# Kernel tuning notes

Measured on AMD Instinct MI355X. Metric: run time of the kernel, lower is better.

The kernel has to match this reference:

```python
import jax, jax.numpy as jnp
import numpy as np

P = 4          # patch_size
LAM = 0.5      # init_lambda
B, C, H, W = 8, 96, 128, 128

def _dct_mat(N):
    # torch_dct unnormalized DCT-II matrix: D[k,n] = 2*cos(pi*(2n+1)k/(2N))
    n = np.arange(N)
    return 2.0 * np.cos(np.pi * (2.0 * n[None, :] + 1.0) * n[:, None] / (2.0 * N))

_D = jnp.asarray(_dct_mat(P), dtype=jnp.float32)
_Di = jnp.asarray(np.linalg.inv(_dct_mat(P)), dtype=jnp.float32)  # exact inverse -> idct(dct(x)) == x

def _dct2(x):
    # DCT-II over last two dims of [..., P, P]
    return jnp.einsum('ij,...jk,lk->...il', _D, x, _D)

def _idct2(x):
    return jnp.einsum('ij,...jk,lk->...il', _Di, x, _Di)

def _conv3x3(x, w, b):
    y = jax.lax.conv_general_dilated(x, w, (1, 1), 'SAME',
                                     dimension_numbers=('NCHW', 'OIHW', 'NCHW'))
    return y + b[None, :, None, None]

def setup_inputs() -> dict:
    key = jax.random.key(0)
    ks = jax.random.split(key, 5)
    std = 1.0 / np.sqrt(C * 9)
    return {
        'input1': jax.random.normal(ks[0], (B, C, H, W), jnp.float32),
        'input2': jax.random.normal(ks[1], (B, C, H, W), jnp.float32),
        'wq': jax.random.normal(ks[2], (C, C, 3, 3), jnp.float32) * std,
        'bq': jnp.zeros((C,), jnp.float32),
        'wk': jax.random.normal(ks[3], (C, C, 3, 3), jnp.float32) * std,
        'bk': jnp.zeros((C,), jnp.float32),
        'wv': jax.random.normal(ks[4], (C, C, 3, 3), jnp.float32) * std,
        'bv': jnp.zeros((C,), jnp.float32),
        'temperature': jnp.ones((1, 1), jnp.float32),
    }

def reference(input1, input2, wq, bq, wk, bk, wv, bv, temperature):
    b, c, h, w = input1.shape
    F_Q = _conv3x3(input1, wq, bq)
    F_K = _conv3x3(input1, wk, bk)
    F_V = _conv3x3(input2, wv, bv)
    hp, wp = h // P, w // P
    # 'b c (h p1) (w p2) -> b c h w p1 p2'
    to_patch = lambda x: x.reshape(b, c, hp, P, wp, P).transpose(0, 1, 2, 4, 3, 5)
    fft_Q = _dct2(to_patch(F_Q))          # [b,c,hp,wp,P,P]
    fft_K = _dct2(to_patch(F_K))
    F1 = jnp.matmul(fft_Q, fft_K)         # per-patch PxP matmul
    L = hp * wp * P * P                   # == h*w
    F1f = F1.reshape(b, c, L)
    Fq = fft_Q.reshape(b, c, L)
    Fk = fft_K.reshape(b, c, L)
    # channel-channel attention: [b,c,L] @ [b,L,c] -> [b,c,c]
    attn = jnp.einsum('bil,bjl->bij', Fq, Fk) * temperature[0, 0]
    attn = jax.nn.softmax(attn, axis=-1)
    Fcfr = jnp.einsum('bij,bjl->bil', attn, F1f).reshape(b, c, hp, wp, P, P)
    Fcfr_out = _idct2(Fcfr)
    # 'b c h w p1 p2 -> b c (h p1) (w p2)'
    Fcfrout = Fcfr_out.transpose(0, 1, 2, 4, 3, 5).reshape(b, c, h, w)
    out1 = jnp.matmul(Fcfrout, F_V)       # batched HxW matmul (H==W)
    Fdfr = F_V - out1 * LAM
    return jnp.matmul(Fcfrout, F_Q) + Fdfr
```

## Files before the change

kernel.cpp:

```cpp
#include <hip/hip_runtime.h>

typedef unsigned short u16;
typedef unsigned int u32;
typedef __bf16 bf16x8 __attribute__((ext_vector_type(8)));
typedef float f32x4 __attribute__((ext_vector_type(4)));
typedef int i32x4 __attribute__((ext_vector_type(4)));

#define BATCH 8
#define CH 96
#define HWSZ 16384
#define PADP (130*130*96)

#define OFF_FQ     0ULL
#define OFF_FK     50331648ULL
#define OFF_GT     50331648ULL
#define OFF_FVN    75497472ULL
#define OFF_PAD1H  100663296ULL
#define OFF_F1W    100663296ULL
#define OFF_PAD1L  126621696ULL
#define OFF_PART   126621696ULL
#define OFF_PAD2   152580096ULL
#define OFF_FCFR   152580096ULL
#define OFF_FVB    178538496ULL
#define OFF_ATTNB  203704320ULL
#define OFF_WQK    203851776ULL
#define OFF_WV     204515328ULL
#define WS_NEED    204681216ULL

__device__ __forceinline__ u16 f2bf(float f) {
    u32 u = __builtin_bit_cast(u32, f);
    u += 0x7fffu + ((u >> 16) & 1u);
    return (u16)(u >> 16);
}
__device__ __forceinline__ float bf2f(u16 h) {
    u32 u = ((u32)h) << 16;
    return __builtin_bit_cast(float, u);
}
__device__ __forceinline__ f32x4 mfma16(i32x4 a, i32x4 b, f32x4 c) {
    return __builtin_amdgcn_mfma_f32_16x16x32_bf16(
        __builtin_bit_cast(bf16x8, a), __builtin_bit_cast(bf16x8, b), c, 0, 0, 0);
}
__device__ __forceinline__ void gl_lds16(const u16* g, u16* l) {
    __builtin_amdgcn_global_load_lds(
        (const __attribute__((address_space(1))) unsigned int*)g,
        (__attribute__((address_space(3))) unsigned int*)l, 16, 0, 0);
}

__global__ __launch_bounds__(256) void k_diag(float* __restrict__ out, int n, float val) {
    for (int i = blockIdx.x * 256 + threadIdx.x; i < n; i += gridDim.x * 256) out[i] = val;
}

__global__ __launch_bounds__(256) void k_zhalo(u16* __restrict__ p) {
    size_t base = (size_t)blockIdx.x * PADP;
    for (int i = threadIdx.x; i < 130 * 96; i += 256) {
        p[base + i] = 0;
        p[base + (size_t)129 * 130 * 96 + i] = 0;
    }
    for (int i = threadIdx.x; i < 128 * 2 * 96; i += 256) {
        int row = i / 192, k = i - row * 192;
        int x = (k < 96) ? 0 : 129, c = (k < 96) ? k : k - 96;
        p[base + ((size_t)(row + 1) * 130 + x) * 96 + c] = 0;
    }
}

__global__ __launch_bounds__(256) void k_trans_split(const float* __restrict__ src,
        u16* __restrict__ dh, u16* __restrict__ dl) {
    __shared__ float tile[96][129];
    int b = blockIdx.x >> 7, y = blockIdx.x & 127;
    const float* s = src + (size_t)b * CH * HWSZ + (size_t)y * 128;
    for (int idx = threadIdx.x; idx < CH * 128; idx += 256) {
        int c = idx >> 7, x = idx & 127;
        tile[c][x] = s[(size_t)c * HWSZ + x];
    }
    __syncthreads();
    size_t obase = ((size_t)(b * 130 + y + 1) * 130 + 1) * 96;
    for (int idx = threadIdx.x; idx < 128 * CH; idx += 256) {
        int x = idx / CH, c = idx - x * CH;
        float v = tile[c][x];
        u16 h = f2bf(v);
        dh[obase + idx] = h;
        if (dl) dl[obase + idx] = f2bf(v - bf2f(h));
    }
}

__global__ __launch_bounds__(128) void k_weights_qk(const float* __restrict__ wq,
        const float* __restrict__ wk, u16* __restrict__ dst) {
    int co = blockIdx.x;
    const float* w = (co < 96) ? wq : wk;
    int cs = (co < 96) ? co : co - 96;
    for (int idx = threadIdx.x; idx < 864; idx += 128) {
        int tap = idx / 96, ci = idx - tap * 96;
        int cic = ci >> 5, g = (ci >> 3) & 3, c7 = ci & 7;
        float v = w[((size_t)cs * 96 + ci) * 9 + tap];
        u16 h = f2bf(v), lo = f2bf(v - bf2f(h));
        size_t s = (size_t)(cic * 9 + tap);
        dst[(((s * 2 + 0) * 4 + g) * 192 + co) * 8 + c7] = h;
        dst[(((s * 2 + 1) * 4 + g) * 192 + co) * 8 + c7] = lo;
    }
}

__global__ __launch_bounds__(128) void k_weights_v(const float* __restrict__ wv,
        u16* __restrict__ dst) {
    int co = blockIdx.x;
    for (int idx = threadIdx.x; idx < 864; idx += 128) {
        int tap = idx / 96, ci = idx - tap * 96;
        int cic = ci >> 5, g = (ci >> 3) & 3, c7 = ci & 7;
        float v = wv[((size_t)co * 96 + ci) * 9 + tap];
        size_t s = (size_t)(cic * 9 + tap);
        dst[((s * 4 + g) * 96 + co) * 8 + c7] = f2bf(v);
    }
}

__global__ __launch_bounds__(256, 3) void k_convqk2(
        const u16* __restrict__ ph, const u16* __restrict__ pl,
        const u16* __restrict__ wqk,
        const float* __restrict__ bq, const float* __restrict__ bk,
        float* __restrict__ fq, float* __restrict__ fk) {
    __shared__ u16 wbuf[2][12288];
    const int tid = threadIdx.x;
    const int b = blockIdx.x >> 7, y = blockIdx.x & 127;
    const int w = tid >> 6, lane = tid & 63, l15 = lane & 15, g = lane >> 4;
    f32x4 acc[2][12];
#pragma unroll
    for (int mf = 0; mf < 2; mf++)
#pragma unroll
        for (int f = 0; f < 12; f++) acc[mf][f] = (f32x4){0.f, 0.f, 0.f, 0.f};

    {
        u16* ldsb = &wbuf[0][0] + (size_t)w * 64 * 8;
#pragma unroll
        for (int j = 0; j < 6; j++)
            gl_lds16(wqk + (size_t)(j * 256 + tid) * 8, ldsb + (size_t)j * 256 * 8);
    }
    __syncthreads();
    for (int s = 0; s < 27; s++) {
        const int cur = s & 1;
        if (s + 1 < 27) {
            const u16* src = wqk + (size_t)(s + 1) * 12288;
            u16* ldsb = &wbuf[cur ^ 1][0] + (size_t)w * 64 * 8;
#pragma unroll
            for (int j = 0; j < 6; j++)
                gl_lds16(src + (size_t)(j * 256 + tid) * 8, ldsb + (size_t)j * 256 * 8);
        }
        const int cic = s / 9, tap = s - cic * 9;
        const int dy = tap / 3 - 1, dx = tap - (tap / 3) * 3 - 1;
        const int ci0 = cic * 32 + g * 8;
        size_t ab = ((size_t)(b * 130 + y + 1 + dy) * 130 + (w * 32 + l15 + 1 + dx)) * 96 + ci0;
        i32x4 ah0 = *(const i32x4*)(ph + ab);
        i32x4 ah1 = *(const i32x4*)(ph + ab + 16 * 96);
        i32x4 al0 = *(const i32x4*)(pl + ab);
        i32x4 al1 = *(const i32x4*)(pl + ab + 16 * 96);
#pragma unroll
        for (int f = 0; f < 12; f++) {
            i32x4 bh = *(const i32x4*)(&wbuf[cur][((0 + g) * 192 + f * 16 + l15) * 8]);
            i32x4 bl = *(const i32x4*)(&wbuf[cur][((4 + g) * 192 + f * 16 + l15) * 8]);
            acc[0][f] = mfma16(ah0, bh, acc[0][f]);
            acc[0][f] = mfma16(ah0, bl, acc[0][f]);
            acc[0][f] = mfma16(al0, bh, acc[0][f]);
            acc[1][f] = mfma16(ah1, bh, acc[1][f]);
            acc[1][f] = mfma16(ah1, bl, acc[1][f]);
            acc[1][f] = mfma16(al1, bh, acc[1][f]);
        }
        __syncthreads();
    }
#pragma unroll
    for (int f = 0; f < 12; f++) {
        const bool isQ = (f < 6);
        const int co = (isQ ? f : f - 6) * 16 + l15;
        const float bb = isQ ? bq[co] : bk[co];
        float* op = isQ ? fq : fk;
#pragma unroll
        for (int mf = 0; mf < 2; mf++) {
            const int xp = w * 32 + mf * 16 + g * 4;
#pragma unroll
            for (int r = 0; r < 4; r++)
                op[((size_t)((b * 128 + y) * 128 + xp + r)) * 96 + co] = acc[mf][f][r] + bb;
        }
    }
}

__global__ __launch_bounds__(256) void k_convv2(
        const u16* __restrict__ p2, const u16* __restrict__ wv,
        const float* __restrict__ bv, u16* __restrict__ fvb) {
    __shared__ u16 vbuf[2][3072];
    const int tid = threadIdx.x;
    const int b = blockIdx.x >> 7, y = blockIdx.x & 127;
    const int w = tid >> 6, lane = tid & 63, l15 = lane & 15, g = lane >> 4;
    f32x4 acc[2][6];
#pragma unroll
    for (int mf = 0; mf < 2; mf++)
#pragma unroll
        for (int f = 0; f < 6; f++) acc[mf][f] = (f32x4){0.f, 0.f, 0.f, 0.f};
    {
        gl_lds16(wv + (size_t)tid * 8, &vbuf[0][0] + (size_t)w * 64 * 8);
        if (w < 2)
            gl_lds16(wv + (size_t)(256 + tid) * 8, &vbuf[0][0] + (size_t)(256 + w * 64) * 8);
    }
    __syncthreads();
    for (int s = 0; s < 27; s++) {
        const int cur = s & 1;
        if (s + 1 < 27) {
            const u16* src = wv + (size_t)(s + 1) * 3072;
            gl_lds16(src + (size_t)tid * 8, &vbuf[cur ^ 1][0] + (size_t)w * 64 * 8);
            if (w < 2)
                gl_lds16(src + (size_t)(256 + tid) * 8, &vbuf[cur ^ 1][0] + (size_t)(256 + w * 64) * 8);
        }
        const int cic = s / 9, tap = s - cic * 9;
        const int dy = tap / 3 - 1, dx = tap - (tap / 3) * 3 - 1;
        const int ci0 = cic * 32 + g * 8;
        size_t ab = ((size_t)(b * 130 + y + 1 + dy) * 130 + (w * 32 + l15 + 1 + dx)) * 96 + ci0;
        i32x4 ah0 = *(const i32x4*)(p2 + ab);
        i32x4 ah1 = *(const i32x4*)(p2 + ab + 16 * 96);
#pragma unroll
        for (int f = 0; f < 6; f++) {
            i32x4 bfr = *(const i32x4*)(&vbuf[cur][(g * 96 + f * 16 + l15) * 8]);
            acc[0][f] = mfma16(ah0, bfr, acc[0][f]);
            acc[1][f] = mfma16(ah1, bfr, acc[1][f]);
        }
        __syncthreads();
    }
#pragma unroll
    for (int f = 0; f < 6; f++) {
        const int co = f * 16 + l15;
        const float bb = bv[co];
#pragma unroll
        for (int mf = 0; mf < 2; mf++) {
            const int xp = w * 32 + mf * 16 + g * 4;
#pragma unroll
            for (int r = 0; r < 4; r++)
                fvb[((size_t)((b * 128 + y) * 128 + xp + r)) * 96 + co] = f2bf(acc[mf][f][r] + bb);
        }
    }
}

__global__ __launch_bounds__(256) void k_patch(
        const float* __restrict__ fq, float* __restrict__ fk, u16* __restrict__ f1w) {
    int blk = blockIdx.x;
    int b = blk >> 6, py = (blk >> 1) & 31, xh = blk & 1;
    int y0 = py * 4;
    for (int it = 0; it < 6; it++) {
        int item = threadIdx.x + it * 256;
        int pxl = item / 96, c = item - pxl * 96;
        int x0 = (xh * 16 + pxl) * 4;
        float A[4][4], Bm[4][4];
        size_t rb[4];
#pragma unroll
        for (int r = 0; r < 4; r++) {
            rb[r] = ((size_t)((b * 128 + y0 + r) * 128 + x0)) * 96 + c;
#pragma unroll
            for (int m = 0; m < 4; m++) {
                A[r][m] = fq[rb[r] + (size_t)m * 96];
                Bm[r][m] = fk[rb[r] + (size_t)m * 96];
            }
        }
        float rsB[4], csB[4], rsA[4], tot = 0.f;
#pragma unroll
        for (int r = 0; r < 4; r++) {
            rsB[r] = Bm[r][0] + Bm[r][1] + Bm[r][2] + Bm[r][3];
            rsA[r] = A[r][0] + A[r][1] + A[r][2] + A[r][3];
            tot += rsB[r];
        }
#pragma unroll
        for (int m = 0; m < 4; m++) csB[m] = Bm[0][m] + Bm[1][m] + Bm[2][m] + Bm[3][m];
#pragma unroll
        for (int r = 0; r < 4; r++)
#pragma unroll
            for (int m = 0; m < 4; m++)
                fk[rb[r] + (size_t)m * 96] = 64.f * Bm[r][m] + 16.f * (rsB[r] + csB[m]) + 4.f * tot;
#pragma unroll
        for (int r = 0; r < 4; r++)
#pragma unroll
            for (int m = 0; m < 4; m++) {
                float ab = A[r][0] * Bm[0][m] + A[r][1] * Bm[1][m]
                         + A[r][2] * Bm[2][m] + A[r][3] * Bm[3][m];
                f1w[rb[r] + (size_t)m * 96] = f2bf(8.f * ab + 2.f * rsA[r] * csB[m]);
            }
    }
}

__global__ __launch_bounds__(256) void k_attn(
        const float* __restrict__ fq, const float* __restrict__ kt,
        float* __restrict__ part) {
    __shared__ float qs[96 * 65];
    __shared__ float ks[96 * 65];
    int b = blockIdx.x >> 6, s = blockIdx.x & 63;
    int l0 = s * 256;
    int tx = threadIdx.x & 15, ty = threadIdx.x >> 4;
    double accD[6][6];
#pragma unroll
    for (int a = 0; a < 6; a++)
#pragma unroll
        for (int bb = 0; bb < 6; bb++) accD[a][bb] = 0.0;
    for (int ch = 0; ch < 4; ch++) {
        __syncthreads();
        for (int idx = threadIdx.x; idx < 1536; idx += 256) {
            int p = idx / 24, c0 = (idx - p * 24) * 4;
            size_t off = ((size_t)b * 16384 + l0 + ch * 64 + p) * 96 + c0;
            f32x4 qv = *(const f32x4*)(fq + off);
            f32x4 kv = *(const f32x4*)(kt + off);
#pragma unroll
            for (int u = 0; u < 4; u++) {
                qs[(c0 + u) * 65 + p] = qv[u];
                ks[(c0 + u) * 65 + p] = kv[u];
            }
        }
        __syncthreads();
        float acc[6][6];
#pragma unroll
        for (int a = 0; a < 6; a++)
#pragma unroll
            for (int bb = 0; bb < 6; bb++) acc[a][bb] = 0.f;
        for (int l = 0; l < 64; l++) {
            float qv[6], kv[6];
#pragma unroll
            for (int a = 0; a < 6; a++) qv[a] = qs[(ty + 16 * a) * 65 + l];
#pragma unroll
            for (int bb = 0; bb < 6; bb++) kv[bb] = ks[(tx + 16 * bb) * 65 + l];
#pragma unroll
            for (int a = 0; a < 6; a++)
#pragma unroll
                for (int bb = 0; bb < 6; bb++) acc[a][bb] += qv[a] * kv[bb];
        }
#pragma unroll
        for (int a = 0; a < 6; a++)
#pragma unroll
            for (int bb = 0; bb < 6; bb++) accD[a][bb] += (double)acc[a][bb];
    }
#pragma unroll
    for (int a = 0; a < 6; a++)
#pragma unroll
        for (int bb = 0; bb < 6; bb++)
            part[((size_t)((b * 64 + s) * 96 + ty + 16 * a)) * 96 + tx + 16 * bb] = (float)accD[a][bb];
}

__global__ __launch_bounds__(128) void k_softmax(
        const float* __restrict__ part, const float* __restrict__ temp,
        u16* __restrict__ attnb) {
    __shared__ float red[128];
    int b = blockIdx.x / 96, i2 = blockIdx.x - b * 96;
    int j2 = threadIdx.x;
    float v = 0.f;
    if (j2 < 96) {
        for (int s = 0; s < 64; s++)
            v += part[((size_t)((b * 64 + s) * 96 + i2)) * 96 + j2];
        v *= temp[0];
    }
    red[j2] = (j2 < 96) ? v : -3.4e38f;
    __syncthreads();
    for (int off = 64; off >= 1; off >>= 1) {
        if (j2 < off) red[j2] = fmaxf(red[j2], red[j2 + off]);
        __syncthreads();
    }
    float mx = red[0];
    __syncthreads();
    float e = (j2 < 96) ? expf(v - mx) : 0.f;
    red[j2] = e;
    __syncthreads();
    for (int off = 64; off >= 1; off >>= 1) {
        if (j2 < off) red[j2] += red[j2 + off];
        __syncthreads();
    }
    float sum = red[0];
    if (j2 < 96) attnb[((size_t)(b * 96) + i2) * 96 + j2] = f2bf(e / sum);
}

__global__ __launch_bounds__(256) void k_gprep(
        const float* __restrict__ fqn, const u16* __restrict__ fvb,
        u16* __restrict__ gt, u16* __restrict__ fvn) {
    __shared__ u16 lg[8 * 32 * 33];
    __shared__ u16 lv[8 * 32 * 33];
    int blk = blockIdx.x;
    int b = blk / 192;
    int r = blk - b * 192;
    int yt = r / 48; r -= yt * 48;
    int xt = r / 12; int cc = r - xt * 12;
    int y0 = yt * 32, x0 = xt * 32, c0 = cc * 8;
    for (int idx = threadIdx.x; idx < 8192; idx += 256) {
        int pix = idx >> 3, cl = idx & 7;
        int yy = pix >> 5, xx = pix & 31;
        size_t off = ((size_t)((b * 128 + y0 + yy) * 128 + x0 + xx)) * 96 + c0 + cl;
        float q = fqn[off];
        float v = bf2f(fvb[off]);
        int la = (cl * 32 + yy) * 33 + xx;
        lg[la] = f2bf(q - 0.5f * v);
        lv[la] = f2bf(v);
    }
    __syncthreads();
    for (int idx = threadIdx.x; idx < 8192; idx += 256) {
        int yy = idx & 31, xl = (idx >> 5) & 31, cl = idx >> 10;
        gt[((size_t)((b * 96 + c0 + cl) * 128 + x0 + xl)) * 128 + y0 + yy] = lg[(cl * 32 + yy) * 33 + xl];
    }
    for (int idx = threadIdx.x; idx < 8192; idx += 256) {
        int xx = idx & 31, yl = (idx >> 5) & 31, cl = idx >> 10;
        fvn[((size_t)((b * 96 + c0 + cl) * 128 + y0 + yl)) * 128 + x0 + xx] = lv[(cl * 32 + yl) * 33 + xx];
    }
}

__global__ __launch_bounds__(256) void k_fcfr2(
        const u16* __restrict__ attnb, const u16* __restrict__ f1w,
        u16* __restrict__ fc) {
    int b = blockIdx.x >> 6, pc = blockIdx.x & 63;
    int lane = threadIdx.x & 63, wv_ = threadIdx.x >> 6;
    int l15 = lane & 15, g = lane >> 4;
    int pbase = pc * 256 + wv_ * 64;
    f32x4 acc[6][4];
#pragma unroll
    for (int m = 0; m < 6; m++)
#pragma unroll
        for (int n = 0; n < 4; n++) acc[m][n] = (f32x4){0.f, 0.f, 0.f, 0.f};
#pragma unroll
    for (int ks = 0; ks < 3; ks++) {
        int k0 = ks * 32 + g * 8;
        i32x4 afr[6];
#pragma unroll
        for (int m = 0; m < 6; m++)
            afr[m] = *(const i32x4*)(attnb + ((size_t)(b * 96 + m * 16 + l15)) * 96 + k0);
#pragma unroll
        for (int n = 0; n < 4; n++) {
            i32x4 bfr = *(const i32x4*)(f1w + ((size_t)(b * 16384 + pbase + n * 16 + l15)) * 96 + k0);
#pragma unroll
            for (int m = 0; m < 6; m++)
                acc[m][n] = mfma16(afr[m], bfr, acc[m][n]);
        }
    }
#pragma unroll
    for (int m = 0; m < 6; m++)
#pragma unroll
        for (int n = 0; n < 4; n++)
#pragma unroll
            for (int r = 0; r < 4; r++) {
                int i2 = m * 16 + g * 4 + r;
                int pix = pbase + n * 16 + l15;
                fc[((size_t)(b * 96 + i2)) * HWSZ + pix] = f2bf(acc[m][n][r]);
            }
}

__global__ __launch_bounds__(256) void k_final(
        const u16* __restrict__ fc, const u16* __restrict__ gt,
        const u16* __restrict__ fvn, float* __restrict__ out) {
    int b = blockIdx.x / 96, c = blockIdx.x - b * 96;
    int lane = threadIdx.x & 63, wv_ = threadIdx.x >> 6;
    int l15 = lane & 15, g = lane >> 4;
    const u16* A = fc + ((size_t)(b * 96 + c)) * HWSZ;
    const u16* Bm = gt + ((size_t)(b * 96 + c)) * HWSZ;
    f32x4 acc[2][8];
#pragma unroll
    for (int mf = 0; mf < 2; mf++)
#pragma unroll
        for (int nf = 0; nf < 8; nf++) acc[mf][nf] = (f32x4){0.f, 0.f, 0.f, 0.f};
#pragma unroll
    for (int kc = 0; kc < 4; kc++) {
        int k0 = kc * 32 + g * 8;
        i32x4 af[2];
#pragma unroll
        for (int mf = 0; mf < 2; mf++)
            af[mf] = *(const i32x4*)(A + (size_t)(wv_ * 32 + mf * 16 + l15) * 128 + k0);
#pragma unroll
        for (int nf = 0; nf < 8; nf++) {
            i32x4 bf = *(const i32x4*)(Bm + (size_t)(nf * 16 + l15) * 128 + k0);
#pragma unroll
            for (int mf = 0; mf < 2; mf++)
                acc[mf][nf] = mfma16(af[mf], bf, acc[mf][nf]);
        }
    }
    const u16* V = fvn + ((size_t)(b * 96 + c)) * HWSZ;
    float* O = out + ((size_t)(b * 96 + c)) * HWSZ;
#pragma unroll
    for (int mf = 0; mf < 2; mf++)
#pragma unroll
        for (int nf = 0; nf < 8; nf++)
#pragma unroll
            for (int r = 0; r < 4; r++) {
                int y = wv_ * 32 + mf * 16 + g * 4 + r;
                int x = nf * 16 + l15;
                O[y * 128 + x] = acc[mf][nf][r] + bf2f(V[y * 128 + x]);
            }
}

extern "C" void kernel_launch(void* const* d_in, const int* in_sizes, int n_in,
                              void* d_out, int out_size, void* d_ws, size_t ws_size,
                              hipStream_t stream) {
    (void)in_sizes; (void)n_in;
    if (ws_size < (size_t)WS_NEED) {
        k_diag<<<2048, 256, 0, stream>>>((float*)d_out, out_size, (float)(ws_size >> 10));
        return;
    }
    const float* in1 = (const float*)d_in[0];
    const float* in2 = (const float*)d_in[1];
    const float* wq  = (const float*)d_in[2];
    const float* bq  = (const float*)d_in[3];
    const float* wk  = (const float*)d_in[4];
    const float* bk  = (const float*)d_in[5];
    const float* wv  = (const float*)d_in[6];
    const float* bv  = (const float*)d_in[7];
    const float* temp = (const float*)d_in[8];
    char* ws = (char*)d_ws;
    float* FQ   = (float*)(ws + OFF_FQ);
    float* FK   = (float*)(ws + OFF_FK);
    u16*  GT    = (u16*)(ws + OFF_GT);
    u16*  FVN   = (u16*)(ws + OFF_FVN);
    u16*  PAD1H = (u16*)(ws + OFF_PAD1H);
    u16*  PAD1L = (u16*)(ws + OFF_PAD1L);
    u16*  PAD2  = (u16*)(ws + OFF_PAD2);
    u16*  F1W   = (u16*)(ws + OFF_F1W);
    float* PART = (float*)(ws + OFF_PART);
    u16*  FCFR  = (u16*)(ws + OFF_FCFR);
    u16*  FVB   = (u16*)(ws + OFF_FVB);
    u16*  ATTNB = (u16*)(ws + OFF_ATTNB);
    u16*  WQK   = (u16*)(ws + OFF_WQK);
    u16*  WV    = (u16*)(ws + OFF_WV);

    k_zhalo<<<24, 256, 0, stream>>>(PAD1H);
    k_trans_split<<<1024, 256, 0, stream>>>(in1, PAD1H, PAD1L);
    k_trans_split<<<1024, 256, 0, stream>>>(in2, PAD2, nullptr);
    k_weights_qk<<<192, 128, 0, stream>>>(wq, wk, WQK);
    k_weights_v<<<96, 128, 0, stream>>>(wv, WV);
    k_convqk2<<<1024, 256, 0, stream>>>(PAD1H, PAD1L, WQK, bq, bk, FQ, FK);
    k_convv2<<<1024, 256, 0, stream>>>(PAD2, WV, bv, FVB);
    k_patch<<<512, 256, 0, stream>>>(FQ, FK, F1W);
    k_attn<<<512, 256, 0, stream>>>(FQ, FK, PART);
    k_softmax<<<768, 128, 0, stream>>>(PART, temp, ATTNB);
    k_gprep<<<1536, 256, 0, stream>>>(FQ, FVB, GT, FVN);
    k_fcfr2<<<512, 256, 0, stream>>>(ATTNB, F1W, FCFR);
    k_final<<<768, 256, 0, stream>>>(FCFR, GT, FVN, (float*)d_out);
}
```

Baseline: 405.4 us.

## Split conv output channels across 8 waves and prefetch next activation fragments

Both conv kernels now launch 512-thread blocks in which waves are split by x-quarter and output-channel half, so each wave holds half as many accumulators. Activation fragments for the next step are loaded into registers one iteration ahead, alongside the LDS weight prefetch. The aim is to lower register pressure, raise occupancy and hide global load latency. In exchange, each activation fragment is loaded by two waves instead of one, and the extra prefetch registers partly offset the accumulator savings.

```diff
diff --git a/kernel.cpp b/kernel.cpp
--- a/kernel.cpp
+++ b/kernel.cpp
@@ -111,7 +111,7 @@
     }
 }
 
-__global__ __launch_bounds__(256, 3) void k_convqk2(
+__global__ __launch_bounds__(512, 4) void k_convqk3(
         const u16* __restrict__ ph, const u16* __restrict__ pl,
         const u16* __restrict__ wqk,
         const float* __restrict__ bq, const float* __restrict__ bk,
@@ -120,40 +120,50 @@
     const int tid = threadIdx.x;
     const int b = blockIdx.x >> 7, y = blockIdx.x & 127;
     const int w = tid >> 6, lane = tid & 63, l15 = lane & 15, g = lane >> 4;
-    f32x4 acc[2][12];
+    const int wx = w & 3, wc = w >> 2;
+    f32x4 acc[2][6];
 #pragma unroll
     for (int mf = 0; mf < 2; mf++)
 #pragma unroll
-        for (int f = 0; f < 12; f++) acc[mf][f] = (f32x4){0.f, 0.f, 0.f, 0.f};
+        for (int f = 0; f < 6; f++) acc[mf][f] = (f32x4){0.f, 0.f, 0.f, 0.f};
 
     {
-        u16* ldsb = &wbuf[0][0] + (size_t)w * 64 * 8;
-#pragma unroll
-        for (int j = 0; j < 6; j++)
-            gl_lds16(wqk + (size_t)(j * 256 + tid) * 8, ldsb + (size_t)j * 256 * 8);
+#pragma unroll
+        for (int j = 0; j < 3; j++)
+            gl_lds16(wqk + (size_t)(tid + j * 512) * 8, &wbuf[0][(size_t)(tid + j * 512) * 8]);
+    }
+    i32x4 ah0, ah1, al0, al1;
+    {
+        size_t ab = ((size_t)(b * 130 + y) * 130 + (wx * 32 + l15)) * 96 + g * 8;
+        ah0 = *(const i32x4*)(ph + ab);
+        ah1 = *(const i32x4*)(ph + ab + 16 * 96);
+        al0 = *(const i32x4*)(pl + ab);
+        al1 = *(const i32x4*)(pl + ab + 16 * 96);
     }
     __syncthreads();
     for (int s = 0; s < 27; s++) {
         const int cur = s & 1;
+        i32x4 nh0, nh1, nl0, nl1;
         if (s + 1 < 27) {
             const u16* src = wqk + (size_t)(s + 1) * 12288;
-            u16* ldsb = &wbuf[cur ^ 1][0] + (size_t)w * 64 * 8;
-#pragma unroll
-            for (int j = 0; j < 6; j++)
-                gl_lds16(src + (size_t)(j * 256 + tid) * 8, ldsb + (size_t)j * 256 * 8);
-        }
-        const int cic = s / 9, tap = s - cic * 9;
-        const int dy = tap / 3 - 1, dx = tap - (tap / 3) * 3 - 1;
-        const int ci0 = cic * 32 + g * 8;
-        size_t ab = ((size_t)(b * 130 + y + 1 + dy) * 130 + (w * 32 + l15 + 1 + dx)) * 96 + ci0;
-        i32x4 ah0 = *(const i32x4*)(ph + ab);
-        i32x4 ah1 = *(const i32x4*)(ph + ab + 16 * 96);
-        i32x4 al0 = *(const i32x4*)(pl + ab);
-        i32x4 al1 = *(const i32x4*)(pl + ab + 16 * 96);
-#pragma unroll
-        for (int f = 0; f < 12; f++) {
-            i32x4 bh = *(const i32x4*)(&wbuf[cur][((0 + g) * 192 + f * 16 + l15) * 8]);
-            i32x4 bl = *(const i32x4*)(&wbuf[cur][((4 + g) * 192 + f * 16 + l15) * 8]);
+#pragma unroll
+            for (int j = 0; j < 3; j++)
+                gl_lds16(src + (size_t)(tid + j * 512) * 8, &wbuf[cur ^ 1][(size_t)(tid + j * 512) * 8]);
+            const int s1 = s + 1;
+            const int cic1 = s1 / 9, tap1 = s1 - cic1 * 9;
+            const int dy1 = tap1 / 3 - 1, dx1 = tap1 - (tap1 / 3) * 3 - 1;
+            size_t ab = ((size_t)(b * 130 + y + 1 + dy1) * 130 + (wx * 32 + l15 + 1 + dx1)) * 96
+                      + cic1 * 32 + g * 8;
+            nh0 = *(const i32x4*)(ph + ab);
+            nh1 = *(const i32x4*)(ph + ab + 16 * 96);
+            nl0 = *(const i32x4*)(pl + ab);
+            nl1 = *(const i32x4*)(pl + ab + 16 * 96);
+        }
+#pragma unroll
+        for (int f = 0; f < 6; f++) {
+            const int cob = wc * 96 + f * 16 + l15;
+            i32x4 bh = *(const i32x4*)(&wbuf[cur][((0 + g) * 192 + cob) * 8]);
+            i32x4 bl = *(const i32x4*)(&wbuf[cur][((4 + g) * 192 + cob) * 8]);
             acc[0][f] = mfma16(ah0, bh, acc[0][f]);
             acc[0][f] = mfma16(ah0, bl, acc[0][f]);
             acc[0][f] = mfma16(al0, bh, acc[0][f]);
@@ -162,16 +172,17 @@
             acc[1][f] = mfma16(al1, bh, acc[1][f]);
         }
         __syncthreads();
-    }
-#pragma unroll
-    for (int f = 0; f < 12; f++) {
-        const bool isQ = (f < 6);
-        const int co = (isQ ? f : f - 6) * 16 + l15;
-        const float bb = isQ ? bq[co] : bk[co];
-        float* op = isQ ? fq : fk;
+        if (s + 1 < 27) { ah0 = nh0; ah1 = nh1; al0 = nl0; al1 = nl1; }
+    }
+    const float* bias = wc ? bk : bq;
+    float* op = wc ? fk : fq;
+#pragma unroll
+    for (int f = 0; f < 6; f++) {
+        const int co = f * 16 + l15;
+        const float bb = bias[co];
 #pragma unroll
         for (int mf = 0; mf < 2; mf++) {
-            const int xp = w * 32 + mf * 16 + g * 4;
+            const int xp = wx * 32 + mf * 16 + g * 4;
 #pragma unroll
             for (int r = 0; r < 4; r++)
                 op[((size_t)((b * 128 + y) * 128 + xp + r)) * 96 + co] = acc[mf][f][r] + bb;
@@ -179,53 +190,59 @@
     }
 }
 
-__global__ __launch_bounds__(256) void k_convv2(
+__global__ __launch_bounds__(512, 4) void k_convv3(
         const u16* __restrict__ p2, const u16* __restrict__ wv,
         const float* __restrict__ bv, u16* __restrict__ fvb) {
     __shared__ u16 vbuf[2][3072];
     const int tid = threadIdx.x;
     const int b = blockIdx.x >> 7, y = blockIdx.x & 127;
     const int w = tid >> 6, lane = tid & 63, l15 = lane & 15, g = lane >> 4;
-    f32x4 acc[2][6];
+    const int wx = w & 3, wc = w >> 2;
+    f32x4 acc[2][3];
 #pragma unroll
     for (int mf = 0; mf < 2; mf++)
 #pragma unroll
-        for (int f = 0; f < 6; f++) acc[mf][f] = (f32x4){0.f, 0.f, 0.f, 0.f};
+        for (int f = 0; f < 3; f++) acc[mf][f] = (f32x4){0.f, 0.f, 0.f, 0.f};
+    if (tid < 384)
+        gl_lds16(wv + (size_t)tid * 8, &vbuf[0][(size_t)tid * 8]);
+    i32x4 ah0, ah1;
     {
-        gl_lds16(wv + (size_t)tid * 8, &vbuf[0][0] + (size_t)w * 64 * 8);
-        if (w < 2)
-            gl_lds16(wv + (size_t)(256 + tid) * 8, &vbuf[0][0] + (size_t)(256 + w * 64) * 8);
+        size_t ab = ((size_t)(b * 130 + y) * 130 + (wx * 32 + l15)) * 96 + g * 8;
+        ah0 = *(const i32x4*)(p2 + ab);
+        ah1 = *(const i32x4*)(p2 + ab + 16 * 96);
     }
     __syncthreads();
     for (int s = 0; s < 27; s++) {
         const int cur = s & 1;
+        i32x4 nh0, nh1;
         if (s + 1 < 27) {
-            const u16* src = wv + (size_t)(s + 1) * 3072;
-            gl_lds16(src + (size_t)tid * 8, &vbuf[cur ^ 1][0] + (size_t)w * 64 * 8);
-            if (w < 2)
-                gl_lds16(src + (size_t)(256 + tid) * 8, &vbuf[cur ^ 1][0] + (size_t)(256 + w * 64) * 8);
-        }
-        const int cic = s / 9, tap = s - cic * 9;
-        const int dy = tap / 3 - 1, dx = tap - (tap / 3) * 3 - 1;
-        const int ci0 = cic * 32 + g * 8;
-        size_t ab = ((size_t)(b * 130 + y + 1 + dy) * 130 + (w * 32 + l15 + 1 + dx)) * 96 + ci0;
-        i32x4 ah0 = *(const i32x4*)(p2 + ab);
-        i32x4 ah1 = *(const i32x4*)(p2 + ab + 16 * 96);
-#pragma unroll
-        for (int f = 0; f < 6; f++) {
-            i32x4 bfr = *(const i32x4*)(&vbuf[cur][(g * 96 + f * 16 + l15) * 8]);
+            if (tid < 384)
+                gl_lds16(wv + (size_t)(s + 1) * 3072 + (size_t)tid * 8, &vbuf[cur ^ 1][(size_t)tid * 8]);
+            const int s1 = s + 1;
+            const int cic1 = s1 / 9, tap1 = s1 - cic1 * 9;
+            const int dy1 = tap1 / 3 - 1, dx1 = tap1 - (tap1 / 3) * 3 - 1;
+            size_t ab = ((size_t)(b * 130 + y + 1 + dy1) * 130 + (wx * 32 + l15 + 1 + dx1)) * 96
+                      + cic1 * 32 + g * 8;
+            nh0 = *(const i32x4*)(p2 + ab);
+            nh1 = *(const i32x4*)(p2 + ab + 16 * 96);
+        }
+#pragma unroll
+        for (int f = 0; f < 3; f++) {
+            const int cob = wc * 48 + f * 16 + l15;
+            i32x4 bfr = *(const i32x4*)(&vbuf[cur][(g * 96 + cob) * 8]);
             acc[0][f] = mfma16(ah0, bfr, acc[0][f]);
             acc[1][f] = mfma16(ah1, bfr, acc[1][f]);
         }
         __syncthreads();
-    }
-#pragma unroll
-    for (int f = 0; f < 6; f++) {
-        const int co = f * 16 + l15;
+        if (s + 1 < 27) { ah0 = nh0; ah1 = nh1; }
+    }
+#pragma unroll
+    for (int f = 0; f < 3; f++) {
+        const int co = wc * 48 + f * 16 + l15;
         const float bb = bv[co];
 #pragma unroll
         for (int mf = 0; mf < 2; mf++) {
-            const int xp = w * 32 + mf * 16 + g * 4;
+            const int xp = wx * 32 + mf * 16 + g * 4;
 #pragma unroll
             for (int r = 0; r < 4; r++)
                 fvb[((size_t)((b * 128 + y) * 128 + xp + r)) * 96 + co] = f2bf(acc[mf][f][r] + bb);
@@ -515,8 +532,8 @@
     k_trans_split<<<1024, 256, 0, stream>>>(in2, PAD2, nullptr);
     k_weights_qk<<<192, 128, 0, stream>>>(wq, wk, WQK);
     k_weights_v<<<96, 128, 0, stream>>>(wv, WV);
-    k_convqk2<<<1024, 256, 0, stream>>>(PAD1H, PAD1L, WQK, bq, bk, FQ, FK);
-    k_convv2<<<1024, 256, 0, stream>>>(PAD2, WV, bv, FVB);
+    k_convqk3<<<1024, 512, 0, stream>>>(PAD1H, PAD1L, WQK, bq, bk, FQ, FK);
+    k_convv3<<<1024, 512, 0, stream>>>(PAD2, WV, bv, FVB);
     k_patch<<<512, 256, 0, stream>>>(FQ, FK, F1W);
     k_attn<<<512, 256, 0, stream>>>(FQ, FK, PART);
     k_softmax<<<768, 128, 0, stream>>>(PART, temp, ATTNB);
```

New measurement: 412.2 us. No clear change (+1.7%).
